# Performance work log

Measured on AMD Instinct MI355X. Metric: run time of the kernel, lower is better.

The kernel has to match this reference:

```python
import jax, jax.numpy as jnp
import numpy as np

N_USERS = 100000
N_ITEMS = 50000
N = N_USERS + N_ITEMS
EMB_DIM = 64
N_LAYERS = 3
NNZ = 6400000
BATCH = 4096


def setup_inputs() -> dict:
    key = jax.random.key(0)
    k = jax.random.split(key, 7)
    user_emb = 0.1 * jax.random.normal(k[0], (N_USERS, EMB_DIM), dtype=jnp.float32)
    item_emb = 0.1 * jax.random.normal(k[1], (N_ITEMS, EMB_DIM), dtype=jnp.float32)
    graph_val = jax.random.uniform(k[2], (NNZ,), dtype=jnp.float32) * 0.05
    graph_src = jax.random.randint(k[3], (NNZ,), 0, N, dtype=jnp.int64) if jax.config.jax_enable_x64 else jax.random.randint(k[3], (NNZ,), 0, N).astype(jnp.int32)
    graph_dst = jax.random.randint(k[4], (NNZ,), 0, N).astype(graph_src.dtype)
    users = jax.random.randint(k[5], (BATCH,), 0, N_USERS).astype(graph_src.dtype)
    items = jax.random.randint(k[6], (BATCH,), 0, N_ITEMS).astype(graph_src.dtype)
    return {"user_emb": user_emb, "item_emb": item_emb, "graph_val": graph_val,
            "graph_src": graph_src, "graph_dst": graph_dst, "users": users, "items": items}


def _spmm(val, src, dst, x):
    # y[src] += val * x[dst]  -- sparse (COO) matrix @ dense
    return jax.ops.segment_sum(val[:, None] * x[dst], src, num_segments=N)


def reference(user_emb, item_emb, graph_val, graph_src, graph_dst, users, items):
    all_emb = jnp.concatenate([user_emb, item_emb], axis=0)  # [N, d]
    acc = all_emb  # running sum over layers (fused mean accumulation)
    x = all_emb
    for _ in range(N_LAYERS):
        x = _spmm(graph_val, graph_src, graph_dst, x)
        acc = acc + x
    light_out = acc / (N_LAYERS + 1)
    all_users = light_out[:N_USERS]
    all_items = light_out[N_USERS:]
    scores = jnp.sum(all_users[users] * all_items[items], axis=1)  # [B]
    return scores
```

## Files before the change

kernel.cpp:

```cpp
#include <hip/hip_runtime.h>


constexpr int N_USERS = 100000;
constexpr int N_ITEMS = 50000;
constexpr int N_NODES = N_USERS + N_ITEMS;
constexpr int EMB = 64;
constexpr int NNZ = 6400000;
constexpr int BATCH = 4096;

constexpr int BSHIFT = 9;
constexpr int BWIDTH = 1 << BSHIFT;
constexpr int NB = (N_NODES + BWIDTH - 1) >> BSHIFT;
constexpr int NBPAD = 512;
constexpr int BSTRIDE = 23500;

constexpr int TILE = 5120;
constexpr int P1_BLOCKS = NNZ / TILE;
constexpr int EPT1 = TILE / 256;

constexpr float QSCALE = 327680.0f;
constexpr float QINV   = 1.0f / 327680.0f;

struct h4 { _Float16 x, y, z, w; };

__global__ void gcur_init_kernel(int* __restrict__ gcur) {
    int i = blockIdx.x * blockDim.x + threadIdx.x;
    if (i < NB) gcur[i] = i * BSTRIDE;
}

__global__ void p1_bin_kernel(const int* __restrict__ src, const int* __restrict__ dst,
                              const float* __restrict__ val, int* __restrict__ gcur,
                              uint2* __restrict__ staging) {
    __shared__ int hist[NBPAD];
    __shared__ int gbase[NBPAD];
    __shared__ int cur[NBPAD];
    __shared__ int sbuf[NBPAD];
    __shared__ int lbase[NBPAD];
    __shared__ uint2 ebuf[TILE];
    int t = threadIdx.x;
    int tile = blockIdx.x * TILE;
    int srcs[EPT1];
    #pragma unroll
    for (int k = 0; k < EPT1; ++k) srcs[k] = src[tile + t + k * 256];
    for (int i = t; i < NBPAD; i += 256) { hist[i] = 0; cur[i] = 0; }
    __syncthreads();
    #pragma unroll
    for (int k = 0; k < EPT1; ++k) atomicAdd(&hist[srcs[k] >> BSHIFT], 1);
    __syncthreads();
    for (int i = t; i < NB; i += 256) {
        int h = hist[i];
        gbase[i] = (h > 0) ? atomicAdd(&gcur[i], h) : 0;
    }
    for (int i = t; i < NBPAD; i += 256) sbuf[i] = hist[i];
    __syncthreads();
    int* pin = sbuf; int* pout = lbase;
    for (int off = 1; off < NBPAD; off <<= 1) {
        for (int i = t; i < NBPAD; i += 256) {
            int v = pin[i];
            if (i >= off) v += pin[i - off];
            pout[i] = v;
        }
        __syncthreads();
        int* tmp = pin; pin = pout; pout = tmp;
    }
    for (int i = t; i < NBPAD; i += 256) lbase[i] = pin[i] - hist[i];
    __syncthreads();
    #pragma unroll
    for (int k = 0; k < EPT1; ++k) {
        int i = tile + t + k * 256;
        int s = srcs[k];
        int b = s >> BSHIFT;
        int c = atomicAdd(&cur[b], 1);
        int d = dst[i];
        float v = val[i];
        unsigned q = (unsigned)(v * QSCALE);
        if (q > 16383u) q = 16383u;
        ebuf[lbase[b] + c] = make_uint2((q << 18) | (unsigned)d, (unsigned)s);
    }
    __syncthreads();
    #pragma unroll
    for (int k = 0; k < EPT1; ++k) {
        int j = t + k * 256;
        uint2 e = ebuf[j];
        int b = (int)(e.y >> BSHIFT);
        unsigned pos = (unsigned)(gbase[b] + (j - lbase[b]));
        if (pos < (unsigned)((b + 1) * BSTRIDE))
            staging[pos] = e;
    }
}

__global__ void bucket_scan_kernel(const int* __restrict__ gcur, int* __restrict__ fbase,
                                   int* __restrict__ roff) {
    __shared__ int sA[NBPAD], sB[NBPAD];
    int t = threadIdx.x;
    int c = (t < NB) ? (gcur[t] - t * BSTRIDE) : 0;
    if (c > BSTRIDE) c = BSTRIDE;
    sA[t] = c;
    __syncthreads();
    int* pin = sA; int* pout = sB;
    for (int off = 1; off < NBPAD; off <<= 1) {
        int v = pin[t];
        if (t >= off) v += pin[t - off];
        pout[t] = v;
        __syncthreads();
        int* tmp = pin; pin = pout; pout = tmp;
    }
    if (t < NB) fbase[t] = pin[t] - c;
    if (t == NB - 1) roff[N_NODES] = pin[t];
}

__global__ void p2_sort_kernel(const int* __restrict__ gcur, const int* __restrict__ fbase,
                               const uint2* __restrict__ staging, unsigned* __restrict__ epack,
                               int* __restrict__ roff) {
    __shared__ int hist[BWIDTH], sA[BWIDTH], sB[BWIDTH], cur[BWIDTH];
    int b = blockIdx.x;
    int t = threadIdx.x;
    int cnt = gcur[b] - b * BSTRIDE;
    if (cnt > BSTRIDE) cnt = BSTRIDE;
    int fb = fbase[b];
    int sbase = b * BSTRIDE;
    for (int i = t; i < BWIDTH; i += 256) hist[i] = 0;
    __syncthreads();
    for (int j = t; j < cnt; j += 256) {
        uint2 e = staging[sbase + j];
        atomicAdd(&hist[e.y & (BWIDTH - 1)], 1);
    }
    __syncthreads();
    for (int i = t; i < BWIDTH; i += 256) sA[i] = hist[i];
    __syncthreads();
    int* pin = sA; int* pout = sB;
    for (int off = 1; off < BWIDTH; off <<= 1) {
        for (int i = t; i < BWIDTH; i += 256) {
            int v = pin[i];
            if (i >= off) v += pin[i - off];
            pout[i] = v;
        }
        __syncthreads();
        int* tmp = pin; pin = pout; pout = tmp;
    }
    for (int i = t; i < BWIDTH; i += 256) {
        int excl = pin[i] - hist[i];
        cur[i] = excl;
        int node = (b << BSHIFT) + i;
        if (node < N_NODES) roff[node] = fb + excl;
    }
    __syncthreads();
    for (int j = t; j < cnt; j += 256) {
        uint2 e = staging[sbase + j];
        int p = atomicAdd(&cur[e.y & (BWIDTH - 1)], 1);
        epack[fb + p] = e.x;
    }
}

__global__ void init_kernel(const float4* __restrict__ ue, const float4* __restrict__ ie,
                            h4* __restrict__ x) {
    int i = blockIdx.x * blockDim.x + threadIdx.x;
    const int total = N_NODES * (EMB / 4);
    if (i >= total) return;
    const int usplit = N_USERS * (EMB / 4);
    float4 v = (i < usplit) ? ue[i] : ie[i - usplit];
    x[i] = h4{(_Float16)v.x, (_Float16)v.y, (_Float16)v.z, (_Float16)v.w};
}

__global__ void gather_init_kernel(const float* __restrict__ ue, const float* __restrict__ ie,
                                   const int* __restrict__ users, const int* __restrict__ items,
                                   float* __restrict__ accb) {
    int gid = blockIdx.x * blockDim.x + threadIdx.x;
    int w = gid >> 6;
    int lane = threadIdx.x & 63;
    if (w >= BATCH * 2) return;
    int b = w >> 1;
    float v;
    if (w & 1) v = ie[(long long)items[b] * EMB + lane];
    else       v = ue[(long long)users[b] * EMB + lane];
    accb[(long long)w * EMB + lane] = v;
}

__global__ void gather_add_kernel(const _Float16* __restrict__ x, const int* __restrict__ users,
                                  const int* __restrict__ items, float* __restrict__ accb) {
    int gid = blockIdx.x * blockDim.x + threadIdx.x;
    int w = gid >> 6;
    int lane = threadIdx.x & 63;
    if (w >= BATCH * 2) return;
    int b = w >> 1;
    int node = (w & 1) ? (N_USERS + items[b]) : users[b];
    accb[(long long)w * EMB + lane] += (float)x[(unsigned)node * EMB + lane];
}

__device__ __forceinline__ float dec_val(unsigned e) {
    return ((float)(e >> 18) + 0.5f) * QINV;
}

__device__ __forceinline__ float row_gather(int beg, int end, int lane,
                                            const unsigned* __restrict__ epack,
                                            const _Float16* __restrict__ x) {
    float s0 = 0.0f, s1 = 0.0f, s2 = 0.0f, s3 = 0.0f;
    for (int j = beg; j < end; j += 64) {
        int idx = j + lane;
        unsigned e = (idx < end) ? epack[idx] : 0u;
        int cnt = min(64, end - j);
        int t = 0;
        #pragma unroll 2
        for (; t + 4 <= cnt; t += 4) {
            unsigned e0 = __shfl(e, t, 64),     e1 = __shfl(e, t + 1, 64);
            unsigned e2 = __shfl(e, t + 2, 64), e3 = __shfl(e, t + 3, 64);
            s0 += dec_val(e0) * (float)x[(e0 & 0x3FFFFu) * EMB + lane];
            s1 += dec_val(e1) * (float)x[(e1 & 0x3FFFFu) * EMB + lane];
            s2 += dec_val(e2) * (float)x[(e2 & 0x3FFFFu) * EMB + lane];
            s3 += dec_val(e3) * (float)x[(e3 & 0x3FFFFu) * EMB + lane];
        }
        for (; t < cnt; ++t) {
            unsigned ee = __shfl(e, t, 64);
            s0 += dec_val(ee) * (float)x[(ee & 0x3FFFFu) * EMB + lane];
        }
    }
    return (s0 + s1) + (s2 + s3);
}

__global__ void spmm_full_kernel(const int* __restrict__ roff, const unsigned* __restrict__ epack,
                                 const _Float16* __restrict__ x, _Float16* __restrict__ y) {
    int row = blockIdx.x * (blockDim.x >> 6) + (threadIdx.x >> 6);
    int lane = threadIdx.x & 63;
    if (row >= N_NODES) return;
    float s = row_gather(roff[row], roff[row + 1], lane, epack, x);
    y[(unsigned)row * EMB + lane] = (_Float16)s;
}

__global__ void spmm_sel_kernel(const int* __restrict__ roff, const unsigned* __restrict__ epack,
                                const _Float16* __restrict__ x, const int* __restrict__ users,
                                const int* __restrict__ items, float* __restrict__ accb) {
    int gid = blockIdx.x * blockDim.x + threadIdx.x;
    int w = gid >> 6;
    int lane = threadIdx.x & 63;
    if (w >= BATCH * 2) return;
    int b = w >> 1;
    int node = (w & 1) ? (N_USERS + items[b]) : users[b];
    float s = row_gather(roff[node], roff[node + 1], lane, epack, x);
    accb[(long long)w * EMB + lane] += s;
}

__global__ void score_kernel(const float* __restrict__ accb, float* __restrict__ out) {
    int gid = blockIdx.x * blockDim.x + threadIdx.x;
    int b = gid >> 6;
    int lane = threadIdx.x & 63;
    if (b >= BATCH) return;
    float a = accb[(long long)(2 * b) * EMB + lane];
    float c = accb[(long long)(2 * b + 1) * EMB + lane];
    float p = a * c;
    #pragma unroll
    for (int off = 32; off > 0; off >>= 1) p += __shfl_down(p, off, 64);
    if (lane == 0) out[b] = p * (1.0f / 16.0f);
}

extern "C" void kernel_launch(void* const* d_in, const int* in_sizes, int n_in,
                              void* d_out, int out_size, void* d_ws, size_t ws_size,
                              hipStream_t stream) {
    const float* user_emb  = (const float*)d_in[0];
    const float* item_emb  = (const float*)d_in[1];
    const float* graph_val = (const float*)d_in[2];
    const int*   graph_src = (const int*)d_in[3];
    const int*   graph_dst = (const int*)d_in[4];
    const int*   users     = (const int*)d_in[5];
    const int*   items     = (const int*)d_in[6];
    float* out = (float*)d_out;

    char* base = (char*)d_ws;
    const size_t STAGE_BYTES = (size_t)BSTRIDE * NB * 8;
    const size_t XBYTES = (size_t)N_NODES * EMB * 2;
    uint2*    staging = (uint2*)base;
    _Float16* A       = (_Float16*)base;
    _Float16* B       = (_Float16*)(base + XBYTES);
    float*    accb    = (float*)(base + 2 * XBYTES);
    unsigned* epack   = (unsigned*)(base + STAGE_BYTES);
    int*      roff    = (int*)(epack + NNZ);
    int*      gcur    = roff + (N_NODES + 1);
    int*      fbase   = gcur + NB;

    const int totalv4 = N_NODES * (EMB / 4);
    const int vblocks = (totalv4 + 255) / 256;
    const int wblocks = (BATCH * 2 * 64) / 256;
    const int sblocks = (N_NODES + 3) / 4;

    gcur_init_kernel<<<(NB + 255) / 256, 256, 0, stream>>>(gcur);
    p1_bin_kernel<<<P1_BLOCKS, 256, 0, stream>>>(graph_src, graph_dst, graph_val,
                                                 gcur, staging);
    bucket_scan_kernel<<<1, NBPAD, 0, stream>>>(gcur, fbase, roff);
    p2_sort_kernel<<<NB, 256, 0, stream>>>(gcur, fbase, staging, epack, roff);

    init_kernel<<<vblocks, 256, 0, stream>>>((const float4*)user_emb,
                                             (const float4*)item_emb, (h4*)A);
    gather_init_kernel<<<wblocks, 256, 0, stream>>>(user_emb, item_emb, users, items, accb);

    spmm_full_kernel<<<sblocks, 256, 0, stream>>>(roff, epack, A, B);
    gather_add_kernel<<<wblocks, 256, 0, stream>>>(B, users, items, accb);

    spmm_full_kernel<<<sblocks, 256, 0, stream>>>(roff, epack, B, A);
    gather_add_kernel<<<wblocks, 256, 0, stream>>>(A, users, items, accb);

    spmm_sel_kernel<<<wblocks, 256, 0, stream>>>(roff, epack, A, users, items, accb);

    score_kernel<<<(BATCH * 64) / 256, 256, 0, stream>>>(accb, out);
}
```

Before: 570.3 us.

## Split wavefront into quarter-waves gathering four fp16 columns per lane

Restructures the SpMM row gather so each 64-lane wavefront processes four edges at once. Each 16-lane quarter loads a full 64-element fp16 row with 8-byte vector loads, and the partial sums are combined at the end with cross-quarter shuffles. The aim is to issue fewer, wider memory instructions and fewer shuffles per edge in a kernel dominated by random row gathers. The cost is extra reduction shuffles, more accumulator registers, and only 16 lanes doing the final stores.

Result: faster. 507.9 us (-10.9%).

```diff
diff --git a/kernel.cpp b/kernel.cpp
--- a/kernel.cpp
+++ b/kernel.cpp
@@ -22,6 +22,7 @@
 constexpr float QINV   = 1.0f / 327680.0f;
 
 struct h4 { _Float16 x, y, z, w; };
+typedef _Float16 half4v __attribute__((ext_vector_type(4)));
 
 __global__ void gcur_init_kernel(int* __restrict__ gcur) {
     int i = blockIdx.x * blockDim.x + threadIdx.x;
@@ -191,30 +192,54 @@
     return ((float)(e >> 18) + 0.5f) * QINV;
 }
 
-__device__ __forceinline__ float row_gather(int beg, int end, int lane,
-                                            const unsigned* __restrict__ epack,
-                                            const _Float16* __restrict__ x) {
-    float s0 = 0.0f, s1 = 0.0f, s2 = 0.0f, s3 = 0.0f;
+__device__ __forceinline__ void row_gather_q(int beg, int end, int lane,
+                                             const unsigned* __restrict__ epack,
+                                             const _Float16* __restrict__ x,
+                                             float acc[4]) {
+    const int sub = lane >> 4;
+    const unsigned li4 = (unsigned)(lane & 15) * 4;
+    float a0 = 0, a1 = 0, a2 = 0, a3 = 0;
+    float b0 = 0, b1 = 0, b2 = 0, b3 = 0;
     for (int j = beg; j < end; j += 64) {
         int idx = j + lane;
         unsigned e = (idx < end) ? epack[idx] : 0u;
         int cnt = min(64, end - j);
         int t = 0;
-        #pragma unroll 2
-        for (; t + 4 <= cnt; t += 4) {
-            unsigned e0 = __shfl(e, t, 64),     e1 = __shfl(e, t + 1, 64);
-            unsigned e2 = __shfl(e, t + 2, 64), e3 = __shfl(e, t + 3, 64);
-            s0 += dec_val(e0) * (float)x[(e0 & 0x3FFFFu) * EMB + lane];
-            s1 += dec_val(e1) * (float)x[(e1 & 0x3FFFFu) * EMB + lane];
-            s2 += dec_val(e2) * (float)x[(e2 & 0x3FFFFu) * EMB + lane];
-            s3 += dec_val(e3) * (float)x[(e3 & 0x3FFFFu) * EMB + lane];
-        }
-        for (; t < cnt; ++t) {
-            unsigned ee = __shfl(e, t, 64);
-            s0 += dec_val(ee) * (float)x[(ee & 0x3FFFFu) * EMB + lane];
-        }
-    }
-    return (s0 + s1) + (s2 + s3);
+        for (; t + 8 <= cnt; t += 8) {
+            unsigned eA = __shfl(e, t + sub, 64);
+            unsigned eB = __shfl(e, t + 4 + sub, 64);
+            half4v hA = *(const half4v*)(x + ((eA & 0x3FFFFu) << 6) + li4);
+            half4v hB = *(const half4v*)(x + ((eB & 0x3FFFFu) << 6) + li4);
+            float vA = dec_val(eA);
+            float vB = dec_val(eB);
+            a0 += vA * (float)hA.x;  a1 += vA * (float)hA.y;
+            a2 += vA * (float)hA.z;  a3 += vA * (float)hA.w;
+            b0 += vB * (float)hB.x;  b1 += vB * (float)hB.y;
+            b2 += vB * (float)hB.z;  b3 += vB * (float)hB.w;
+        }
+        if (t + 4 <= cnt) {
+            unsigned eA = __shfl(e, t + sub, 64);
+            half4v hA = *(const half4v*)(x + ((eA & 0x3FFFFu) << 6) + li4);
+            float vA = dec_val(eA);
+            a0 += vA * (float)hA.x;  a1 += vA * (float)hA.y;
+            a2 += vA * (float)hA.z;  a3 += vA * (float)hA.w;
+            t += 4;
+        }
+        if (t < cnt) {
+            unsigned eA = __shfl(e, t + sub, 64);
+            bool ok = (t + sub) < cnt;
+            float vA = ok ? dec_val(eA) : 0.0f;
+            half4v hA = *(const half4v*)(x + ((eA & 0x3FFFFu) << 6) + li4);
+            a0 += vA * (float)hA.x;  a1 += vA * (float)hA.y;
+            a2 += vA * (float)hA.z;  a3 += vA * (float)hA.w;
+        }
+    }
+    a0 += b0; a1 += b1; a2 += b2; a3 += b3;
+    a0 += __shfl_xor(a0, 16, 64);  a0 += __shfl_xor(a0, 32, 64);
+    a1 += __shfl_xor(a1, 16, 64);  a1 += __shfl_xor(a1, 32, 64);
+    a2 += __shfl_xor(a2, 16, 64);  a2 += __shfl_xor(a2, 32, 64);
+    a3 += __shfl_xor(a3, 16, 64);  a3 += __shfl_xor(a3, 32, 64);
+    acc[0] = a0; acc[1] = a1; acc[2] = a2; acc[3] = a3;
 }
 
 __global__ void spmm_full_kernel(const int* __restrict__ roff, const unsigned* __restrict__ epack,
@@ -222,8 +247,12 @@
     int row = blockIdx.x * (blockDim.x >> 6) + (threadIdx.x >> 6);
     int lane = threadIdx.x & 63;
     if (row >= N_NODES) return;
-    float s = row_gather(roff[row], roff[row + 1], lane, epack, x);
-    y[(unsigned)row * EMB + lane] = (_Float16)s;
+    float acc[4];
+    row_gather_q(roff[row], roff[row + 1], lane, epack, x, acc);
+    if (lane < 16) {
+        half4v h = {(_Float16)acc[0], (_Float16)acc[1], (_Float16)acc[2], (_Float16)acc[3]};
+        *(half4v*)(y + ((unsigned)row << 6) + (unsigned)lane * 4) = h;
+    }
 }
 
 __global__ void spmm_sel_kernel(const int* __restrict__ roff, const unsigned* __restrict__ epack,
@@ -235,8 +264,14 @@
     if (w >= BATCH * 2) return;
     int b = w >> 1;
     int node = (w & 1) ? (N_USERS + items[b]) : users[b];
-    float s = row_gather(roff[node], roff[node + 1], lane, epack, x);
-    accb[(long long)w * EMB + lane] += s;
+    float acc[4];
+    row_gather_q(roff[node], roff[node + 1], lane, epack, x, acc);
+    if (lane < 16) {
+        float4* p = (float4*)(accb + ((long long)w << 6) + lane * 4);
+        float4 c = *p;
+        c.x += acc[0]; c.y += acc[1]; c.z += acc[2]; c.w += acc[3];
+        *p = c;
+    }
 }
 
 __global__ void score_kernel(const float* __restrict__ accb, float* __restrict__ out) {
```
